# Kernel optimization log

Measured on AMD Instinct MI355X. Metric: run time of the kernel, lower is better.

## Reference

```python
import jax, jax.numpy as jnp
import numpy as np

N = 100000
E = 3200000
IN_C, HID_C, OUT_C = 128, 128, 64


def setup_inputs() -> dict:
    key = jax.random.key(0)
    k_x, k_e, k_w1, k_w2 = jax.random.split(key, 4)
    x = jax.random.normal(k_x, (N, IN_C), dtype=jnp.float32)
    edge_index = jax.random.randint(k_e, (2, E), 0, N, dtype=jnp.int64)
    # GCNConv uses Glorot-init weight [in, out] and zero bias
    W1 = jax.random.normal(k_w1, (IN_C, HID_C), dtype=jnp.float32) * (1.0 / np.sqrt(IN_C))
    b1 = jnp.zeros((HID_C,), dtype=jnp.float32)
    W2 = jax.random.normal(k_w2, (HID_C, OUT_C), dtype=jnp.float32) * (1.0 / np.sqrt(HID_C))
    b2 = jnp.zeros((OUT_C,), dtype=jnp.float32)
    return {"x": x, "edge_index": edge_index, "W1": W1, "b1": b1, "W2": W2, "b2": b2}


def _gcn_norm(edge_index, n_nodes):
    """Add self-loops and compute symmetric normalization coefficients."""
    loop = jnp.arange(n_nodes, dtype=edge_index.dtype)
    src = jnp.concatenate([edge_index[0], loop])  # [E+N]
    dst = jnp.concatenate([edge_index[1], loop])  # [E+N]
    ones = jnp.ones(src.shape[0], dtype=jnp.float32)
    deg = jax.ops.segment_sum(ones, dst, num_segments=n_nodes)  # in-degree w/ self loops
    dinv = jnp.where(deg > 0, jax.lax.rsqrt(deg), 0.0)
    norm = dinv[src] * dinv[dst]  # [E+N]
    return src, dst, norm


def _gcn_conv(x, W, b, src, dst, norm, n_nodes):
    h = x @ W                                   # [N, out] dense transform first (PyG order)
    msg = norm[:, None] * h[src]                # gather + scale  [E+N, out]
    out = jax.ops.segment_sum(msg, dst, num_segments=n_nodes)  # scatter-add
    return out + b


def reference(x, edge_index, W1, b1, W2, b2):
    src, dst, norm = _gcn_norm(edge_index, N)
    h = _gcn_conv(x, W1, b1, src, dst, norm, N)
    h = jax.nn.relu(h)
    out = _gcn_conv(h, W2, b2, src, dst, norm, N)
    return out
```

## Files before the change

kernel.cpp:

```cpp
#include <hip/hip_runtime.h>

typedef unsigned int u32;
typedef unsigned short u16;
typedef unsigned long long u64;
typedef __bf16 bf16x8 __attribute__((ext_vector_type(8)));
typedef float floatx4 __attribute__((ext_vector_type(4)));
typedef u32 u32x2 __attribute__((ext_vector_type(2)));
typedef u32 u32x4 __attribute__((ext_vector_type(4)));


__device__ __forceinline__ u16 f2bf(float f) {
  u32 u = __float_as_uint(f);
  u += 0x7fffu + ((u >> 16) & 1u);
  return (u16)(u >> 16);
}
__device__ __forceinline__ float bflo(u32 v) { return __uint_as_float(v << 16); }
__device__ __forceinline__ float bfhi(u32 v) { return __uint_as_float(v & 0xffff0000u); }

#define SLICE_SH 10
#define SL (1 << SLICE_SH)
#define MAXNS 128
#define NBBIN 1280

__device__ __forceinline__ void gemm1_body(const float* __restrict__ X,
                                           const float* __restrict__ W,
                                           u16* __restrict__ Y, int nrows,
                                           int bid, u16* Wt) {
  constexpr int K = 128, OUT = 128, NT = 8, LDW = 136;
  int tid = threadIdx.x;
  for (int idx = tid; idx < K * OUT; idx += 256) {
    int k = idx >> 7, n = idx & 127;
    Wt[n * LDW + k] = f2bf(W[idx]);
  }
  __syncthreads();
  int lane = tid & 63, wave = tid >> 6;
  int quad = lane >> 4, low = lane & 15;
  int mBase = bid * 64 + wave * 16;
  int m = mBase + low;
  int ml = (m < nrows) ? m : (nrows - 1);
  floatx4 acc[NT];
#pragma unroll
  for (int i = 0; i < NT; i++) acc[i] = (floatx4)0.0f;
#pragma unroll
  for (int kb = 0; kb < 4; kb++) {
    int k0 = kb * 32 + quad * 8;
    floatx4 p0 = *(const floatx4*)(X + (size_t)ml * K + k0);
    floatx4 p1 = *(const floatx4*)(X + (size_t)ml * K + k0 + 4);
    union { bf16x8 v; u16 s[8]; } au;
#pragma unroll
    for (int j = 0; j < 4; j++) { au.s[j] = f2bf(p0[j]); au.s[4 + j] = f2bf(p1[j]); }
#pragma unroll
    for (int nt = 0; nt < NT; nt++) {
      bf16x8 b = *(const bf16x8*)(&Wt[(nt * 16 + low) * LDW + k0]);
      acc[nt] = __builtin_amdgcn_mfma_f32_16x16x32_bf16(au.v, b, acc[nt], 0, 0, 0);
    }
  }
#pragma unroll
  for (int nt = 0; nt < NT; nt++) {
    int col = nt * 16 + low;
#pragma unroll
    for (int r = 0; r < 4; r++) {
      int row = mBase + quad * 4 + r;
      if (row < nrows) Y[(size_t)row * OUT + col] = f2bf(acc[nt][r]);
    }
  }
}

__device__ __forceinline__ void bin_body(const int* __restrict__ ei,
                                         int* __restrict__ scur,
                                         u64* __restrict__ stA, u64* __restrict__ stB,
                                         int splitS, int cap, int e, int ns,
                                         int bid, int* hist, int* curs) {
  int per = (e + NBBIN - 1) / NBBIN;
  int e0 = bid * per;
  int e1 = e0 + per; if (e1 > e) e1 = e;
  for (int t = threadIdx.x; t < ns; t += 256) hist[t] = 0;
  __syncthreads();
  for (int i = e0 + threadIdx.x; i < e1; i += 256) {
    int d = ei[e + i];
    atomicAdd(&hist[d >> SLICE_SH], 1);
  }
  __syncthreads();
  for (int t = threadIdx.x; t < ns; t += 256)
    curs[t] = atomicAdd(&scur[t], hist[t]);
  __syncthreads();
  int i = e0 + threadIdx.x;
  for (; i + 768 < e1; i += 1024) {
    int d[4], s[4], pos[4];
#pragma unroll
    for (int p = 0; p < 4; p++) {
      int ii = i + 256 * p;
      s[p] = ei[ii]; d[p] = ei[e + ii];
    }
#pragma unroll
    for (int p = 0; p < 4; p++) pos[p] = atomicAdd(&curs[d[p] >> SLICE_SH], 1);
#pragma unroll
    for (int p = 0; p < 4; p++) {
      int sl = d[p] >> SLICE_SH;
      u64* st = (sl < splitS) ? stA + (size_t)sl * cap : stB + (size_t)(sl - splitS) * cap;
      st[pos[p]] = ((u64)(u32)d[p] << 32) | (u32)s[p];
    }
  }
  for (; i < e1; i += 256) {
    int s = ei[i], d = ei[e + i];
    int sl = d >> SLICE_SH;
    u64* st = (sl < splitS) ? stA + (size_t)sl * cap : stB + (size_t)(sl - splitS) * cap;
    st[atomicAdd(&curs[sl], 1)] = ((u64)(u32)d << 32) | (u32)s;
  }
}

__global__ __launch_bounds__(256) void gemm1_bin(const float* __restrict__ X,
                                                 const float* __restrict__ W1,
                                                 u16* __restrict__ Y, int nrows, int nbGemm,
                                                 const int* __restrict__ ei,
                                                 int* __restrict__ scur,
                                                 u64* __restrict__ stA, u64* __restrict__ stB,
                                                 int splitS, int cap, int e, int ns) {
  __shared__ __attribute__((aligned(16))) char smbuf[128 * 136 * 2];
  int id = blockIdx.x;
  int small = (NBBIN < nbGemm) ? NBBIN : nbGemm;
  int isBin, bid;
  if (id < 2 * small) { isBin = !(id & 1); bid = id >> 1; }
  else { bid = small + (id - 2 * small); isBin = (NBBIN > nbGemm); }
  if (isBin) {
    int* hist = (int*)smbuf;
    int* curs = hist + MAXNS;
    bin_body(ei, scur, stA, stB, splitS, cap, e, ns, bid, hist, curs);
  } else {
    gemm1_body(X, W1, Y, nrows, bid, (u16*)smbuf);
  }
}

__global__ __launch_bounds__(1024) void fill_slice3(const u64* __restrict__ stA,
                                                    const u64* __restrict__ stB,
                                                    const int* __restrict__ scur,
                                                    int* __restrict__ rp,
                                                    float* __restrict__ dinv,
                                                    int* __restrict__ csr,
                                                    int splitS, int cap, int n, int ns) {
  __shared__ int cnt[SL];
  __shared__ int part[SL];
  __shared__ int sb[MAXNS];
  const int s = blockIdx.x;
  const int base = s << SLICE_SH;
  const int tid = threadIdx.x;
  cnt[tid] = 0;
  if (tid < MAXNS) sb[tid] = (tid < ns) ? scur[tid] : 0;
  __syncthreads();
  for (int off = 1; off < MAXNS; off <<= 1) {
    int v = 0;
    if (tid < MAXNS && tid >= off) v = sb[tid - off];
    __syncthreads();
    if (tid < MAXNS) sb[tid] += v;
    __syncthreads();
  }
  const int csrLo = s ? sb[s - 1] : 0;
  const int m = sb[s] - csrLo;
  if (s == ns - 1 && tid == 0) rp[n] = sb[ns - 1];
  const u64* st = (s < splitS) ? stA + (size_t)s * cap : stB + (size_t)(s - splitS) * cap;
  {
    int i = tid;
    for (; i + 7168 < m; i += 8192) {
      int b[8];
#pragma unroll
      for (int p = 0; p < 8; p++) b[p] = (int)(st[i + 1024 * p] >> 32) & (SL - 1);
#pragma unroll
      for (int p = 0; p < 8; p++) atomicAdd(&cnt[b[p]], 1);
    }
    for (; i < m; i += 1024)
      atomicAdd(&cnt[(int)(st[i] >> 32) & (SL - 1)], 1);
  }
  __syncthreads();
  int c0 = cnt[tid];
  part[tid] = c0;
  __syncthreads();
  for (int off = 1; off < SL; off <<= 1) {
    int t = (tid >= off) ? part[tid - off] : 0;
    __syncthreads();
    part[tid] += t;
    __syncthreads();
  }
  int p0 = csrLo + (tid ? part[tid - 1] : 0);
  __syncthreads();
  cnt[tid] = p0;
  int d0 = base + tid;
  if (d0 < n) { rp[d0] = p0; dinv[d0] = rsqrtf((float)(c0 + 1)); }
  __syncthreads();
  {
    int i = tid;
    for (; i + 7168 < m; i += 8192) {
      u64 pr[8]; int pos[8];
#pragma unroll
      for (int p = 0; p < 8; p++) pr[p] = st[i + 1024 * p];
#pragma unroll
      for (int p = 0; p < 8; p++)
        pos[p] = atomicAdd(&cnt[(int)(pr[p] >> 32) & (SL - 1)], 1);
#pragma unroll
      for (int p = 0; p < 8; p++) csr[pos[p]] = (int)(pr[p] & 0xffffffffu);
    }
    for (; i < m; i += 1024) {
      u64 pr = st[i];
      int pos = atomicAdd(&cnt[(int)(pr >> 32) & (SL - 1)], 1);
      csr[pos] = (int)(pr & 0xffffffffu);
    }
  }
}

__global__ __launch_bounds__(256) void agg128_g2(const u32* __restrict__ H,
                                                 const int* __restrict__ rp,
                                                 const int* __restrict__ cs,
                                                 const float* __restrict__ dinv,
                                                 const float* __restrict__ b1,
                                                 const float* __restrict__ W2,
                                                 u16* __restrict__ h2, int n) {
  __shared__ u16 Wt[64 * 136];
  __shared__ u16 Arow[16 * 136];
  const int tid = threadIdx.x;
  for (int idx = tid; idx < 128 * 64; idx += 256) {
    int k = idx >> 6, nn = idx & 63;
    Wt[nn * 136 + k] = f2bf(W2[idx]);
  }
  const int nodeBase = blockIdx.x * 4;
  const int wave = tid >> 6, lane = tid & 63;
  int node = nodeBase + wave;
  int nodeC = (node < n) ? node : (n - 1);
  int e4 = lane >> 4, c = lane & 15;
  int s0 = rp[nodeC], s1 = rp[nodeC + 1];
  float a[8] = {0.f, 0.f, 0.f, 0.f, 0.f, 0.f, 0.f, 0.f};
  for (int base = s0; base < s1; base += 64) {
    int nb = s1 - base; if (nb > 64) nb = 64;
    int src = 0; float dv = 0.f;
    if (lane < nb) { src = cs[base + lane]; dv = dinv[src]; }
    for (int j = 0; j < nb; j += 16) {
      u32x4 v[4]; float w[4];
#pragma unroll
      for (int p = 0; p < 4; p++) {
        int idx = j + 4 * p + e4;
        int sj = __shfl(src, idx);
        w[p] = __shfl(dv, idx);
        v[p] = *(const u32x4*)(H + (size_t)sj * 64 + 4 * c);
      }
#pragma unroll
      for (int p = 0; p < 4; p++) {
#pragma unroll
        for (int k = 0; k < 4; k++) {
          a[2 * k]     += w[p] * bflo(v[p][k]);
          a[2 * k + 1] += w[p] * bfhi(v[p][k]);
        }
      }
    }
  }
#pragma unroll
  for (int k = 0; k < 8; k++) {
    a[k] += __shfl_xor(a[k], 16);
    a[k] += __shfl_xor(a[k], 32);
  }
  float ds = dinv[nodeC];
  u32x4 vs = *(const u32x4*)(H + (size_t)nodeC * 64 + 4 * c);
  floatx4 bb0 = *(const floatx4*)(b1 + 8 * c);
  floatx4 bb1 = *(const floatx4*)(b1 + 8 * c + 4);
  float r[8];
#pragma unroll
  for (int k = 0; k < 4; k++) {
    r[2 * k]     = ds * (a[2 * k]     + ds * bflo(vs[k]));
    r[2 * k + 1] = ds * (a[2 * k + 1] + ds * bfhi(vs[k]));
  }
#pragma unroll
  for (int k = 0; k < 4; k++) { r[k] += bb0[k]; r[4 + k] += bb1[k]; }
#pragma unroll
  for (int k = 0; k < 8; k++) r[k] = fmaxf(r[k], 0.f);
  if (e4 == 0) {
    union { u16 s[8]; u32x4 v; } pk;
#pragma unroll
    for (int k = 0; k < 8; k++) pk.s[k] = f2bf(r[k]);
    *(u32x4*)&Arow[wave * 136 + 8 * c] = pk.v;
  }
  __syncthreads();
  const int quad = e4, low = c;
  floatx4 acc = (floatx4)0.0f;
#pragma unroll
  for (int kb = 0; kb < 4; kb++) {
    int k0 = kb * 32 + quad * 8;
    bf16x8 af = *(const bf16x8*)&Arow[low * 136 + k0];
    bf16x8 bf = *(const bf16x8*)&Wt[(wave * 16 + low) * 136 + k0];
    acc = __builtin_amdgcn_mfma_f32_16x16x32_bf16(af, bf, acc, 0, 0, 0);
  }
  if (quad == 0) {
#pragma unroll
    for (int rI = 0; rI < 4; rI++) {
      int row = nodeBase + rI;
      if (row < n) h2[(size_t)row * 64 + wave * 16 + low] = f2bf(acc[rI]);
    }
  }
}

__global__ __launch_bounds__(256) void agg_64(const u16* __restrict__ Hu,
                                              const int* __restrict__ rp,
                                              const int* __restrict__ cs,
                                              const float* __restrict__ dinv,
                                              const float* __restrict__ b2,
                                              float* __restrict__ out, int n) {
  const u32* H = (const u32*)Hu;
  int node = blockIdx.x * 4 + (threadIdx.x >> 6);
  if (node >= n) return;
  int lane = threadIdx.x & 63;
  int e4 = lane >> 4, c = lane & 15;
  int s0 = rp[node], s1 = rp[node + 1];
  float a[4] = {0.f, 0.f, 0.f, 0.f};
  for (int base = s0; base < s1; base += 64) {
    int nb = s1 - base; if (nb > 64) nb = 64;
    int src = 0; float dv = 0.f;
    if (lane < nb) { src = cs[base + lane]; dv = dinv[src]; }
    for (int j = 0; j < nb; j += 16) {
      u32x2 v[4]; float w[4];
#pragma unroll
      for (int p = 0; p < 4; p++) {
        int idx = j + 4 * p + e4;
        int sj = __shfl(src, idx);
        w[p] = __shfl(dv, idx);
        v[p] = *(const u32x2*)(H + (size_t)sj * 32 + 2 * c);
      }
#pragma unroll
      for (int p = 0; p < 4; p++) {
        a[0] += w[p] * bflo(v[p].x); a[1] += w[p] * bfhi(v[p].x);
        a[2] += w[p] * bflo(v[p].y); a[3] += w[p] * bfhi(v[p].y);
      }
    }
  }
#pragma unroll
  for (int k = 0; k < 4; k++) {
    a[k] += __shfl_xor(a[k], 16);
    a[k] += __shfl_xor(a[k], 32);
  }
  float ds = dinv[node];
  u32x2 vs = *(const u32x2*)(H + (size_t)node * 32 + 2 * c);
  floatx4 bf = *(const floatx4*)(b2 + 4 * c);
  if (e4 == 0) {
    floatx4 o;
    o[0] = ds * (a[0] + ds * bflo(vs.x)) + bf[0];
    o[1] = ds * (a[1] + ds * bfhi(vs.x)) + bf[1];
    o[2] = ds * (a[2] + ds * bflo(vs.y)) + bf[2];
    o[3] = ds * (a[3] + ds * bfhi(vs.y)) + bf[3];
    *(floatx4*)(out + (size_t)node * 64 + 4 * c) = o;
  }
}


extern "C" void kernel_launch(void* const* d_in, const int* in_sizes, int n_in,
                              void* d_out, int out_size, void* d_ws, size_t ws_size,
                              hipStream_t stream) {
  const float* x  = (const float*)d_in[0];
  const int*   ei = (const int*)d_in[1];
  const float* W1 = (const float*)d_in[2];
  const float* b1 = (const float*)d_in[3];
  const float* W2 = (const float*)d_in[4];
  const float* b2 = (const float*)d_in[5];
  const int N = in_sizes[0] / 128;
  const int E = in_sizes[1] / 2;
  const int NS = (N + SL - 1) >> SLICE_SH;

  int CAP = (E + NS - 1) / NS;
  CAP += CAP / 8;
  size_t doutSlots = ((size_t)out_size * 4) / 8;
  int SPLIT = (int)(doutSlots / (size_t)CAP);
  if (SPLIT > NS) SPLIT = NS;

  auto al = [](size_t v) { return (v + 255) & ~(size_t)255; };
  char* ws = (char*)d_ws;
  size_t o = 0;
  int*   scur  = (int*)(ws + o);  o += 512;
  int*   rp    = (int*)(ws + o);  o += al((size_t)(N + 1) * 4);
  float* dinv  = (float*)(ws + o); o += al((size_t)N * 4);
  int*   csr   = (int*)(ws + o);  o += al((size_t)E * 4);
  u16*   h     = (u16*)(ws + o);  o += al((size_t)N * 128 * 2);
  u16*   h2    = (u16*)(ws + o);  o += al((size_t)N * 128 * 2);
  u64* stA = (u64*)d_out;
  u64* stB = (u64*)h2;

  const int nbGemm = (N + 63) / 64;

  hipMemsetAsync(scur, 0, 512, stream);
  gemm1_bin<<<NBBIN + nbGemm, 256, 0, stream>>>(x, W1, h, N, nbGemm,
                                                ei, scur, stA, stB, SPLIT, CAP, E, NS);
  fill_slice3<<<NS, 1024, 0, stream>>>(stA, stB, scur, rp, dinv, csr, SPLIT, CAP, N, NS);
  agg128_g2<<<(N + 3) / 4, 256, 0, stream>>>((const u32*)h, rp, csr, dinv, b1, W2, h2, N);
  agg_64<<<(N + 3) / 4, 256, 0, stream>>>(h2, rp, csr, dinv, b2, (float*)d_out, N);
}
```

Before: 384.7 us.

## Split layer-1 aggregation by column groups per XCD and separate second GEMM

The first GEMM now writes its output in a column-group-major layout, with 8 groups of 16 bf16 columns. The layer-1 aggregation is split so that each block handles one group, chosen from the low 3 bits of blockIdx. The apparent intent is that each XCD gathers from a 3.2 MB slice of H that can stay in its local L2 instead of the full 25.6 MB matrix. Each wave walks 8 nodes and prefetches the next node's edge list, and the fused layer-2 MFMA becomes a separate gemm2 kernel that reads the grouped h1 staged in the output buffer. This costs one extra launch plus an extra write and read of h1, and every edge list is now read eight times.

```diff
diff --git a/kernel.cpp b/kernel.cpp
--- a/kernel.cpp
+++ b/kernel.cpp
@@ -57,11 +57,10 @@
   }
 #pragma unroll
   for (int nt = 0; nt < NT; nt++) {
-    int col = nt * 16 + low;
 #pragma unroll
     for (int r = 0; r < 4; r++) {
       int row = mBase + quad * 4 + r;
-      if (row < nrows) Y[(size_t)row * OUT + col] = f2bf(acc[nt][r]);
+      if (row < nrows) Y[((size_t)nt * nrows + row) * 16 + low] = f2bf(acc[nt][r]);
     }
   }
 }
@@ -206,90 +205,110 @@
   }
 }
 
-__global__ __launch_bounds__(256) void agg128_g2(const u32* __restrict__ H,
-                                                 const int* __restrict__ rp,
-                                                 const int* __restrict__ cs,
-                                                 const float* __restrict__ dinv,
-                                                 const float* __restrict__ b1,
-                                                 const float* __restrict__ W2,
-                                                 u16* __restrict__ h2, int n) {
-  __shared__ u16 Wt[64 * 136];
-  __shared__ u16 Arow[16 * 136];
-  const int tid = threadIdx.x;
+__global__ __launch_bounds__(256) void agg128_xcd(const u32* __restrict__ P,
+                                                  const int* __restrict__ rp,
+                                                  const int* __restrict__ cs,
+                                                  const float* __restrict__ dinv,
+                                                  const float* __restrict__ b1,
+                                                  u32* __restrict__ h1g,
+                                                  int n) {
+  const int g = blockIdx.x & 7;
+  const int nb0 = (blockIdx.x >> 3) * 32;
+  const int lane = threadIdx.x & 63;
+  const int wave = threadIdx.x >> 6;
+  const int epos = lane >> 3, p8 = lane & 7;
+  const u32* __restrict__ Pg = P + (size_t)g * n * 8;
+  u32* __restrict__ Hg = h1g + (size_t)g * n * 8;
+  const float bb0 = b1[g * 16 + 2 * p8];
+  const float bb1 = b1[g * 16 + 2 * p8 + 1];
+  int v = nb0 + wave * 8;
+  int s0 = 0, s1 = 0, src = 0; float dv = 0.f;
+  if (v < n) {
+    s0 = rp[v]; s1 = rp[v + 1];
+    int nb = s1 - s0; if (nb > 64) nb = 64;
+    if (lane < nb) { src = __builtin_nontemporal_load(cs + s0 + lane); dv = dinv[src]; }
+  }
+  for (int t = 0; t < 8; t++, v++) {
+    if (v >= n) break;
+    int ns0 = 0, ns1 = 0, nsrc = 0; float ndv = 0.f;
+    if (t < 7 && v + 1 < n) {
+      ns0 = rp[v + 1]; ns1 = rp[v + 2];
+      int nb = ns1 - ns0; if (nb > 64) nb = 64;
+      if (lane < nb) { nsrc = __builtin_nontemporal_load(cs + ns0 + lane); ndv = dinv[nsrc]; }
+    }
+    float a0 = 0.f, a1 = 0.f;
+    int base = s0, csrc = src; float cdv = dv;
+    for (;;) {
+      int nbb = s1 - base; if (nbb > 64) nbb = 64;
+      for (int j = 0; j < nbb; j += 8) {
+        int idx = j + epos;
+        int sj = __shfl(csrc, idx);
+        float w = __shfl(cdv, idx);
+        u32 val = Pg[(size_t)sj * 8 + p8];
+        a0 += w * bflo(val);
+        a1 += w * bfhi(val);
+      }
+      base += 64;
+      if (base >= s1) break;
+      int nb2 = s1 - base; if (nb2 > 64) nb2 = 64;
+      csrc = 0; cdv = 0.f;
+      if (lane < nb2) { csrc = __builtin_nontemporal_load(cs + base + lane); cdv = dinv[csrc]; }
+    }
+#pragma unroll
+    for (int off = 8; off < 64; off <<= 1) {
+      a0 += __shfl_xor(a0, off);
+      a1 += __shfl_xor(a1, off);
+    }
+    float ds = dinv[v];
+    u32 sv = Pg[(size_t)v * 8 + p8];
+    float r0 = ds * (a0 + ds * bflo(sv)) + bb0;
+    float r1 = ds * (a1 + ds * bfhi(sv)) + bb1;
+    r0 = fmaxf(r0, 0.f); r1 = fmaxf(r1, 0.f);
+    if (epos == 0) {
+      u32 pk = (u32)f2bf(r0) | ((u32)f2bf(r1) << 16);
+      __builtin_nontemporal_store(pk, Hg + (size_t)v * 8 + p8);
+    }
+    s0 = ns0; s1 = ns1; src = nsrc; dv = ndv;
+  }
+}
+
+__global__ __launch_bounds__(256) void gemm2(const u16* __restrict__ h1g,
+                                             const float* __restrict__ W2,
+                                             u16* __restrict__ h2, int nrows) {
+  constexpr int LDW = 136;
+  __shared__ u16 Wt[64 * LDW];
+  int tid = threadIdx.x;
   for (int idx = tid; idx < 128 * 64; idx += 256) {
     int k = idx >> 6, nn = idx & 63;
-    Wt[nn * 136 + k] = f2bf(W2[idx]);
-  }
-  const int nodeBase = blockIdx.x * 4;
-  const int wave = tid >> 6, lane = tid & 63;
-  int node = nodeBase + wave;
-  int nodeC = (node < n) ? node : (n - 1);
-  int e4 = lane >> 4, c = lane & 15;
-  int s0 = rp[nodeC], s1 = rp[nodeC + 1];
-  float a[8] = {0.f, 0.f, 0.f, 0.f, 0.f, 0.f, 0.f, 0.f};
-  for (int base = s0; base < s1; base += 64) {
-    int nb = s1 - base; if (nb > 64) nb = 64;
-    int src = 0; float dv = 0.f;
-    if (lane < nb) { src = cs[base + lane]; dv = dinv[src]; }
-    for (int j = 0; j < nb; j += 16) {
-      u32x4 v[4]; float w[4];
-#pragma unroll
-      for (int p = 0; p < 4; p++) {
-        int idx = j + 4 * p + e4;
-        int sj = __shfl(src, idx);
-        w[p] = __shfl(dv, idx);
-        v[p] = *(const u32x4*)(H + (size_t)sj * 64 + 4 * c);
-      }
-#pragma unroll
-      for (int p = 0; p < 4; p++) {
-#pragma unroll
-        for (int k = 0; k < 4; k++) {
-          a[2 * k]     += w[p] * bflo(v[p][k]);
-          a[2 * k + 1] += w[p] * bfhi(v[p][k]);
-        }
-      }
-    }
-  }
-#pragma unroll
-  for (int k = 0; k < 8; k++) {
-    a[k] += __shfl_xor(a[k], 16);
-    a[k] += __shfl_xor(a[k], 32);
-  }
-  float ds = dinv[nodeC];
-  u32x4 vs = *(const u32x4*)(H + (size_t)nodeC * 64 + 4 * c);
-  floatx4 bb0 = *(const floatx4*)(b1 + 8 * c);
-  floatx4 bb1 = *(const floatx4*)(b1 + 8 * c + 4);
-  float r[8];
-#pragma unroll
-  for (int k = 0; k < 4; k++) {
-    r[2 * k]     = ds * (a[2 * k]     + ds * bflo(vs[k]));
-    r[2 * k + 1] = ds * (a[2 * k + 1] + ds * bfhi(vs[k]));
-  }
-#pragma unroll
-  for (int k = 0; k < 4; k++) { r[k] += bb0[k]; r[4 + k] += bb1[k]; }
-#pragma unroll
-  for (int k = 0; k < 8; k++) r[k] = fmaxf(r[k], 0.f);
-  if (e4 == 0) {
-    union { u16 s[8]; u32x4 v; } pk;
-#pragma unroll
-    for (int k = 0; k < 8; k++) pk.s[k] = f2bf(r[k]);
-    *(u32x4*)&Arow[wave * 136 + 8 * c] = pk.v;
-  }
-  __syncthreads();
-  const int quad = e4, low = c;
-  floatx4 acc = (floatx4)0.0f;
+    Wt[nn * LDW + k] = f2bf(W2[idx]);
+  }
+  __syncthreads();
+  int lane = tid & 63, wave = tid >> 6;
+  int quad = lane >> 4, low = lane & 15;
+  int mBase = blockIdx.x * 64 + wave * 16;
+  int m = mBase + low;
+  int ml = (m < nrows) ? m : (nrows - 1);
+  floatx4 acc[4];
+#pragma unroll
+  for (int i = 0; i < 4; i++) acc[i] = (floatx4)0.0f;
 #pragma unroll
   for (int kb = 0; kb < 4; kb++) {
-    int k0 = kb * 32 + quad * 8;
-    bf16x8 af = *(const bf16x8*)&Arow[low * 136 + k0];
-    bf16x8 bf = *(const bf16x8*)&Wt[(wave * 16 + low) * 136 + k0];
-    acc = __builtin_amdgcn_mfma_f32_16x16x32_bf16(af, bf, acc, 0, 0, 0);
-  }
-  if (quad == 0) {
-#pragma unroll
-    for (int rI = 0; rI < 4; rI++) {
-      int row = nodeBase + rI;
-      if (row < n) h2[(size_t)row * 64 + wave * 16 + low] = f2bf(acc[rI]);
+    int kq = kb * 32 + quad * 8;
+    int gI = 2 * kb + (quad >> 1);
+    int off = (quad & 1) * 8;
+    bf16x8 a = *(const bf16x8*)(h1g + ((size_t)gI * nrows + ml) * 16 + off);
+#pragma unroll
+    for (int nt = 0; nt < 4; nt++) {
+      bf16x8 b = *(const bf16x8*)(&Wt[(nt * 16 + low) * LDW + kq]);
+      acc[nt] = __builtin_amdgcn_mfma_f32_16x16x32_bf16(a, b, acc[nt], 0, 0, 0);
+    }
+  }
+#pragma unroll
+  for (int nt = 0; nt < 4; nt++) {
+#pragma unroll
+    for (int r = 0; r < 4; r++) {
+      int row = mBase + quad * 4 + r;
+      if (row < nrows) h2[(size_t)row * 64 + nt * 16 + low] = f2bf(acc[nt][r]);
     }
   }
 }
@@ -376,6 +395,7 @@
   u16*   h2    = (u16*)(ws + o);  o += al((size_t)N * 128 * 2);
   u64* stA = (u64*)d_out;
   u64* stB = (u64*)h2;
+  u16* h1g = (u16*)d_out;
 
   const int nbGemm = (N + 63) / 64;
 
@@ -383,6 +403,8 @@
   gemm1_bin<<<NBBIN + nbGemm, 256, 0, stream>>>(x, W1, h, N, nbGemm,
                                                 ei, scur, stA, stB, SPLIT, CAP, E, NS);
   fill_slice3<<<NS, 1024, 0, stream>>>(stA, stB, scur, rp, dinv, csr, SPLIT, CAP, N, NS);
-  agg128_g2<<<(N + 3) / 4, 256, 0, stream>>>((const u32*)h, rp, csr, dinv, b1, W2, h2, N);
+  agg128_xcd<<<8 * ((N + 31) / 32), 256, 0, stream>>>((const u32*)h, rp, csr, dinv, b1,
+                                                      (u32*)h1g, N);
+  gemm2<<<(N + 63) / 64, 256, 0, stream>>>(h1g, W2, h2, N);
   agg_64<<<(N + 3) / 4, 256, 0, stream>>>(h2, rp, csr, dinv, b2, (float*)d_out, N);
 }
```

Result: slower. 664.2 us (+72.7%).
